# Performance work log

Hardware: AMD Instinct MI355X
Metric: run time of the kernel (lower is better)

Reference implementation:

```python
import jax, jax.numpy as jnp
import numpy as np
import math

B, H, S, D = 8, 16, 1024, 64

def setup_inputs() -> dict:
    key = jax.random.key(0)
    kq, kk, kv = jax.random.split(key, 3)
    Q = jax.random.normal(kq, (B, H, S, D), dtype=jnp.float32)
    K = jax.random.normal(kk, (B, H, S, D), dtype=jnp.float32)
    V = jax.random.normal(kv, (B, H, S, D), dtype=jnp.float32)
    return {"Q": Q, "K": K, "V": V}

def reference(Q, K, V):
    d_k = K.shape[-1]
    # [B,H,S,S] attention scores
    score = jnp.einsum('bhqd,bhkd->bhqk', Q, K) / math.sqrt(d_k)
    attn = jax.nn.softmax(score, axis=-1)
    return jnp.einsum('bhqk,bhkd->bhqd', attn, V)
```

## Files before the change

### kernel.cpp

```cpp
#include <hip/hip_runtime.h>
#include <hip/hip_bf16.h>
#include <math.h>


#define S_ 1024
#define D_ 64
#define BQ 256
#define KVT 64
#define NTILE (S_ / KVT)
#define TILE_SHORTS (KVT * D_)

typedef __attribute__((ext_vector_type(8))) short bf16x8;
typedef __attribute__((ext_vector_type(4))) float f32x4;

#if __has_builtin(__builtin_amdgcn_exp2f)
#define EXP2F(x) __builtin_amdgcn_exp2f(x)
#else
#define EXP2F(x) exp2f(x)
#endif

__device__ __forceinline__ short f2bf(float f) {
    union { __hip_bfloat16 h; short s; } u;
    u.h = __float2bfloat16(f);
    return u.s;
}

__device__ __forceinline__ unsigned int pkbf(float a, float b) {
    unsigned int ua = __float_as_uint(a) + 0x8000u;
    unsigned int ub = __float_as_uint(b) + 0x8000u;
    return __builtin_amdgcn_perm(ub, ua, 0x07060302u);
}

__launch_bounds__(256)
__global__ void prepass_kernel(const float* __restrict__ K, const float* __restrict__ V,
                               short* __restrict__ Kb, short* __restrict__ Vb) {
    __shared__ __align__(16) short VtL[D_][72];
    const int tile = blockIdx.x, bh = blockIdx.y;
    const int tid = threadIdx.x;
    const int kv0 = tile * KVT;
    const size_t base = (size_t)bh * (S_ * D_);
    const float* Kp = K + base;
    const float* Vp = V + base;
    short* Kt = Kb + ((size_t)bh * NTILE + tile) * TILE_SHORTS;
    short* Vt = Vb + ((size_t)bh * NTILE + tile) * TILE_SHORTS;

    {
        const int c4 = tid & 15, g = tid >> 4;
        #pragma unroll
        for (int i = 0; i < 2; ++i) {
            const int kp = g + 16 * i;
            #pragma unroll
            for (int j = 0; j < 4; ++j) {
                const int d = c4 + 16 * j;
                float v0 = Vp[(size_t)(kv0 + 2 * kp) * D_ + d];
                float v1 = Vp[(size_t)(kv0 + 2 * kp + 1) * D_ + d];
                short2 vs; vs.x = f2bf(v0); vs.y = f2bf(v1);
                *(short2*)&VtL[d][2 * kp] = vs;
            }
        }
    }
    #pragma unroll
    for (int i = 0; i < 2; ++i) {
        const int s = tid + i * 256;
        const int mb = s >> 7, c = (s >> 6) & 1, lane = s & 63;
        const int quad = lane >> 4, l16 = lane & 15;
        const float* src = Kp + (size_t)(kv0 + mb * 16 + l16) * D_ + c * 32 + quad * 8;
        float4 a = *(const float4*)src;
        float4 b = *(const float4*)(src + 4);
        bf16x8 f;
        f[0]=f2bf(a.x); f[1]=f2bf(a.y); f[2]=f2bf(a.z); f[3]=f2bf(a.w);
        f[4]=f2bf(b.x); f[5]=f2bf(b.y); f[6]=f2bf(b.z); f[7]=f2bf(b.w);
        *(bf16x8*)&Kt[s * 8] = f;
    }
    __syncthreads();
    #pragma unroll
    for (int i = 0; i < 2; ++i) {
        const int s = tid + i * 256;
        const int t = s >> 7, c = (s >> 6) & 1, lane = s & 63;
        const int quad = lane >> 4, l16 = lane & 15;
        bf16x8 f = *(const bf16x8*)&VtL[t * 16 + l16][c * 32 + quad * 8];
        *(bf16x8*)&Vt[s * 8] = f;
    }
}

__launch_bounds__(256, 2)
__global__ void sdpa_kernel(const float* __restrict__ Q,
                            const short* __restrict__ Kb,
                            const short* __restrict__ Vb,
                            float* __restrict__ O) {
    __shared__ __align__(16) short Pfrag[4][4][1024];

    const int b   = blockIdx.x;
    const int bh  = (b & 7) | ((b >> 5) << 3);
    const int q0  = ((b >> 3) & 3) * BQ;
    const int tid = threadIdx.x;
    const int w = tid >> 6, lane = tid & 63;
    const int quad = lane >> 4, l16 = lane & 15;

    const size_t base = (size_t)bh * (S_ * D_);
    const float* Qp = Q + base;
    float*       Op = O + base;
    const short* Kg = Kb + (size_t)bh * NTILE * TILE_SHORTS;
    const short* Vg = Vb + (size_t)bh * NTILE * TILE_SHORTS;

    const float qs = 0.18033688011112042f;
    bf16x8 qfrag[4][2];
    #pragma unroll
    for (int nb = 0; nb < 4; ++nb) {
        const int qrow = q0 + w * 64 + nb * 16 + l16;
        #pragma unroll
        for (int c = 0; c < 2; ++c) {
            const float* src = Qp + (size_t)qrow * D_ + c * 32 + quad * 8;
            float4 a = *(const float4*)(src);
            float4 bb = *(const float4*)(src + 4);
            bf16x8 f;
            f[0]=f2bf(a.x*qs);  f[1]=f2bf(a.y*qs);  f[2]=f2bf(a.z*qs);  f[3]=f2bf(a.w*qs);
            f[4]=f2bf(bb.x*qs); f[5]=f2bf(bb.y*qs); f[6]=f2bf(bb.z*qs); f[7]=f2bf(bb.w*qs);
            qfrag[nb][c] = f;
        }
    }

    bf16x8 ones;
    #pragma unroll
    for (int i = 0; i < 8; ++i) ones[i] = (short)0x3F80;

    f32x4 l_acc[4];
    f32x4 o_acc[4][4];
    #pragma unroll
    for (int nb = 0; nb < 4; ++nb) {
        l_acc[nb] = (f32x4)0.f;
        #pragma unroll
        for (int t4 = 0; t4 < 4; ++t4)
            o_acc[nb][t4] = (f32x4)0.f;
    }

    auto body = [&](bf16x8 (&kfc)[4][2], bf16x8 (&kfn)[4][2], int t) {
        bf16x8 vf[4][2];
        {
            const short* vt = Vg + (size_t)t * TILE_SHORTS;
            #pragma unroll
            for (int mb = 0; mb < 4; ++mb) {
                vf[mb][0] = *(const bf16x8*)(vt + ((mb * 2 + 0) * 64 + lane) * 8);
                vf[mb][1] = *(const bf16x8*)(vt + ((mb * 2 + 1) * 64 + lane) * 8);
            }
        }
        if (t + 1 < NTILE) {
            const short* kt = Kg + (size_t)(t + 1) * TILE_SHORTS;
            #pragma unroll
            for (int mb = 0; mb < 4; ++mb) {
                kfn[mb][0] = *(const bf16x8*)(kt + ((mb * 2 + 0) * 64 + lane) * 8);
                kfn[mb][1] = *(const bf16x8*)(kt + ((mb * 2 + 1) * 64 + lane) * 8);
            }
        }

        #pragma unroll
        for (int nb = 0; nb < 4; ++nb) {
            f32x4 st[4];
            #pragma unroll
            for (int mb = 0; mb < 4; ++mb) {
                f32x4 acc = (f32x4)0.f;
                acc = __builtin_amdgcn_mfma_f32_16x16x32_bf16(kfc[mb][0], qfrag[nb][0], acc, 0, 0, 0);
                acc = __builtin_amdgcn_mfma_f32_16x16x32_bf16(kfc[mb][1], qfrag[nb][1], acc, 0, 0, 0);
                st[mb] = acc;
            }

            #pragma unroll
            for (int mb = 0; mb < 4; ++mb) {
                float p0 = EXP2F(st[mb][0]);
                float p1 = EXP2F(st[mb][1]);
                float p2 = EXP2F(st[mb][2]);
                float p3 = EXP2F(st[mb][3]);
                uint2 pk;
                pk.x = pkbf(p0, p1);
                pk.y = pkbf(p2, p3);
                const int c  = mb >> 1;
                const int qp = (mb & 1) * 2 + (quad >> 1);
                const int j0 = (quad & 1) * 4;
                *(uint2*)&Pfrag[w][nb][(c * 64 + qp * 16 + l16) * 8 + j0] = pk;
            }
            bf16x8 pf0 = *(const bf16x8*)&Pfrag[w][nb][(0 * 64 + lane) * 8];
            bf16x8 pf1 = *(const bf16x8*)&Pfrag[w][nb][(1 * 64 + lane) * 8];

            l_acc[nb] = __builtin_amdgcn_mfma_f32_16x16x32_bf16(pf0, ones, l_acc[nb], 0, 0, 0);
            l_acc[nb] = __builtin_amdgcn_mfma_f32_16x16x32_bf16(pf1, ones, l_acc[nb], 0, 0, 0);

            #pragma unroll
            for (int t4 = 0; t4 < 4; ++t4) {
                f32x4 acc = o_acc[nb][t4];
                acc = __builtin_amdgcn_mfma_f32_16x16x32_bf16(pf0, vf[t4][0], acc, 0, 0, 0);
                acc = __builtin_amdgcn_mfma_f32_16x16x32_bf16(pf1, vf[t4][1], acc, 0, 0, 0);
                o_acc[nb][t4] = acc;
            }
        }
    };

    bf16x8 kfA[4][2], kfB[4][2];
    #pragma unroll
    for (int mb = 0; mb < 4; ++mb) {
        kfA[mb][0] = *(const bf16x8*)(Kg + ((mb * 2 + 0) * 64 + lane) * 8);
        kfA[mb][1] = *(const bf16x8*)(Kg + ((mb * 2 + 1) * 64 + lane) * 8);
    }

    #pragma unroll 1
    for (int tt = 0; tt < NTILE; tt += 2) {
        body(kfA, kfB, tt);
        body(kfB, kfA, tt + 1);
    }

    #pragma unroll
    for (int nb = 0; nb < 4; ++nb) {
        #pragma unroll
        for (int r = 0; r < 4; ++r) {
            const float inv = 1.0f / l_acc[nb][r];
            const int row = q0 + w * 64 + nb * 16 + quad * 4 + r;
            #pragma unroll
            for (int t4 = 0; t4 < 4; ++t4)
                Op[(size_t)row * D_ + t4 * 16 + l16] = o_acc[nb][t4][r] * inv;
        }
    }
}

extern "C" void kernel_launch(void* const* d_in, const int* in_sizes, int n_in,
                              void* d_out, int out_size, void* d_ws, size_t ws_size,
                              hipStream_t stream) {
    const float* Q = (const float*)d_in[0];
    const float* K = (const float*)d_in[1];
    const float* V = (const float*)d_in[2];
    float* O = (float*)d_out;

    const size_t tensor_shorts = (size_t)128 * NTILE * TILE_SHORTS;
    short* Kb = (short*)d_ws;
    short* Vb = Kb + tensor_shorts;

    dim3 pgrid(NTILE, 8 * 16);
    prepass_kernel<<<pgrid, dim3(256), 0, stream>>>(K, V, Kb, Vb);

    sdpa_kernel<<<dim3(512), dim3(256), 0, stream>>>(Q, Kb, Vb, O);
}
```

Baseline: 164.0 us.

## Switch attention to 32x32x16 MFMA with in-register P transpose via permlane32 swap

Moves the attention kernel from 16x16x32 to 32x32x16 bf16 MFMA tiles and re-lays out the prepacked K/V fragments to match. The P matrix is reshaped into the PV operand layout in registers with permlane32 swaps, removing the LDS round trip through Pfrag and the extra MFMA that computed row sums. Row sums are now accumulated with scalar adds and combined across half-waves at the end. It also drops the double-buffered K prefetch, so K and V for each tile are loaded at the start of that tile's iteration, which may expose more load latency.

```diff
diff --git a/kernel.cpp b/kernel.cpp
--- a/kernel.cpp
+++ b/kernel.cpp
@@ -11,7 +11,8 @@
 #define TILE_SHORTS (KVT * D_)
 
 typedef __attribute__((ext_vector_type(8))) short bf16x8;
-typedef __attribute__((ext_vector_type(4))) float f32x4;
+typedef __attribute__((ext_vector_type(16))) float f32x16;
+typedef __attribute__((ext_vector_type(4))) unsigned int ui4;
 
 #if __has_builtin(__builtin_amdgcn_exp2f)
 #define EXP2F(x) __builtin_amdgcn_exp2f(x)
@@ -29,6 +30,20 @@
     unsigned int ua = __float_as_uint(a) + 0x8000u;
     unsigned int ub = __float_as_uint(b) + 0x8000u;
     return __builtin_amdgcn_perm(ub, ua, 0x07060302u);
+}
+
+__device__ __forceinline__ void swap32(unsigned int x, unsigned int y,
+                                       unsigned int& lo, unsigned int& hi) {
+#if __has_builtin(__builtin_amdgcn_permlane32_swap)
+    auto r = __builtin_amdgcn_permlane32_swap(x, y, false, false);
+    lo = r[0]; hi = r[1];
+#else
+    const int h = (threadIdx.x >> 5) & 1;
+    unsigned int xs = (unsigned int)__shfl_xor((int)x, 32);
+    unsigned int ys = (unsigned int)__shfl_xor((int)y, 32);
+    lo = h ? ys : x;
+    hi = h ? y : xs;
+#endif
 }
 
 __launch_bounds__(256)
@@ -62,9 +77,9 @@
     #pragma unroll
     for (int i = 0; i < 2; ++i) {
         const int s = tid + i * 256;
-        const int mb = s >> 7, c = (s >> 6) & 1, lane = s & 63;
-        const int quad = lane >> 4, l16 = lane & 15;
-        const float* src = Kp + (size_t)(kv0 + mb * 16 + l16) * D_ + c * 32 + quad * 8;
+        const int mb = s >> 8, c = (s >> 6) & 3, lane = s & 63;
+        const int l32 = lane & 31, h = lane >> 5;
+        const float* src = Kp + (size_t)(kv0 + mb * 32 + l32) * D_ + 16 * c + 8 * h;
         float4 a = *(const float4*)src;
         float4 b = *(const float4*)(src + 4);
         bf16x8 f;
@@ -76,9 +91,9 @@
     #pragma unroll
     for (int i = 0; i < 2; ++i) {
         const int s = tid + i * 256;
-        const int t = s >> 7, c = (s >> 6) & 1, lane = s & 63;
-        const int quad = lane >> 4, l16 = lane & 15;
-        bf16x8 f = *(const bf16x8*)&VtL[t * 16 + l16][c * 32 + quad * 8];
+        const int nd = s >> 8, c = (s >> 6) & 3, lane = s & 63;
+        const int l32 = lane & 31, h = lane >> 5;
+        bf16x8 f = *(const bf16x8*)&VtL[nd * 32 + l32][16 * c + 8 * h];
         *(bf16x8*)&Vt[s * 8] = f;
     }
 }
@@ -88,14 +103,12 @@
                             const short* __restrict__ Kb,
                             const short* __restrict__ Vb,
                             float* __restrict__ O) {
-    __shared__ __align__(16) short Pfrag[4][4][1024];
-
     const int b   = blockIdx.x;
     const int bh  = (b & 7) | ((b >> 5) << 3);
     const int q0  = ((b >> 3) & 3) * BQ;
     const int tid = threadIdx.x;
     const int w = tid >> 6, lane = tid & 63;
-    const int quad = lane >> 4, l16 = lane & 15;
+    const int l32 = lane & 31, h = lane >> 5;
 
     const size_t base = (size_t)bh * (S_ * D_);
     const float* Qp = Q + base;
@@ -104,13 +117,13 @@
     const short* Vg = Vb + (size_t)bh * NTILE * TILE_SHORTS;
 
     const float qs = 0.18033688011112042f;
-    bf16x8 qfrag[4][2];
-    #pragma unroll
-    for (int nb = 0; nb < 4; ++nb) {
-        const int qrow = q0 + w * 64 + nb * 16 + l16;
-        #pragma unroll
-        for (int c = 0; c < 2; ++c) {
-            const float* src = Qp + (size_t)qrow * D_ + c * 32 + quad * 8;
+    bf16x8 qfrag[2][4];
+    #pragma unroll
+    for (int nb = 0; nb < 2; ++nb) {
+        const int qrow = q0 + w * 64 + nb * 32 + l32;
+        #pragma unroll
+        for (int c = 0; c < 4; ++c) {
+            const float* src = Qp + (size_t)qrow * D_ + 16 * c + 8 * h;
             float4 a = *(const float4*)(src);
             float4 bb = *(const float4*)(src + 4);
             bf16x8 f;
@@ -120,102 +133,92 @@
         }
     }
 
-    bf16x8 ones;
-    #pragma unroll
-    for (int i = 0; i < 8; ++i) ones[i] = (short)0x3F80;
-
-    f32x4 l_acc[4];
-    f32x4 o_acc[4][4];
-    #pragma unroll
-    for (int nb = 0; nb < 4; ++nb) {
-        l_acc[nb] = (f32x4)0.f;
-        #pragma unroll
-        for (int t4 = 0; t4 < 4; ++t4)
-            o_acc[nb][t4] = (f32x4)0.f;
-    }
-
-    auto body = [&](bf16x8 (&kfc)[4][2], bf16x8 (&kfn)[4][2], int t) {
-        bf16x8 vf[4][2];
-        {
-            const short* vt = Vg + (size_t)t * TILE_SHORTS;
-            #pragma unroll
-            for (int mb = 0; mb < 4; ++mb) {
-                vf[mb][0] = *(const bf16x8*)(vt + ((mb * 2 + 0) * 64 + lane) * 8);
-                vf[mb][1] = *(const bf16x8*)(vt + ((mb * 2 + 1) * 64 + lane) * 8);
-            }
-        }
-        if (t + 1 < NTILE) {
-            const short* kt = Kg + (size_t)(t + 1) * TILE_SHORTS;
-            #pragma unroll
-            for (int mb = 0; mb < 4; ++mb) {
-                kfn[mb][0] = *(const bf16x8*)(kt + ((mb * 2 + 0) * 64 + lane) * 8);
-                kfn[mb][1] = *(const bf16x8*)(kt + ((mb * 2 + 1) * 64 + lane) * 8);
-            }
-        }
-
-        #pragma unroll
-        for (int nb = 0; nb < 4; ++nb) {
-            f32x4 st[4];
-            #pragma unroll
-            for (int mb = 0; mb < 4; ++mb) {
-                f32x4 acc = (f32x4)0.f;
-                acc = __builtin_amdgcn_mfma_f32_16x16x32_bf16(kfc[mb][0], qfrag[nb][0], acc, 0, 0, 0);
-                acc = __builtin_amdgcn_mfma_f32_16x16x32_bf16(kfc[mb][1], qfrag[nb][1], acc, 0, 0, 0);
+    float l_half[2] = {0.f, 0.f};
+    f32x16 o_acc[2][2];
+    #pragma unroll
+    for (int nb = 0; nb < 2; ++nb)
+        #pragma unroll
+        for (int nd = 0; nd < 2; ++nd)
+            o_acc[nb][nd] = (f32x16)0.f;
+
+    #pragma unroll 1
+    for (int t = 0; t < NTILE; ++t) {
+        const short* kt = Kg + (size_t)t * TILE_SHORTS;
+        const short* vt = Vg + (size_t)t * TILE_SHORTS;
+        bf16x8 kf[2][4], vf[2][4];
+        #pragma unroll
+        for (int mb = 0; mb < 2; ++mb)
+            #pragma unroll
+            for (int c = 0; c < 4; ++c)
+                kf[mb][c] = *(const bf16x8*)(kt + (((mb * 4 + c) * 64) + lane) * 8);
+        #pragma unroll
+        for (int nd = 0; nd < 2; ++nd)
+            #pragma unroll
+            for (int c = 0; c < 4; ++c)
+                vf[nd][c] = *(const bf16x8*)(vt + (((nd * 4 + c) * 64) + lane) * 8);
+
+        #pragma unroll
+        for (int nb = 0; nb < 2; ++nb) {
+            f32x16 st[2];
+            #pragma unroll
+            for (int mb = 0; mb < 2; ++mb) {
+                f32x16 acc = (f32x16)0.f;
+                #pragma unroll
+                for (int c = 0; c < 4; ++c)
+                    acc = __builtin_amdgcn_mfma_f32_32x32x16_bf16(kf[mb][c], qfrag[nb][c], acc, 0, 0, 0);
                 st[mb] = acc;
             }
 
-            #pragma unroll
-            for (int mb = 0; mb < 4; ++mb) {
-                float p0 = EXP2F(st[mb][0]);
-                float p1 = EXP2F(st[mb][1]);
-                float p2 = EXP2F(st[mb][2]);
-                float p3 = EXP2F(st[mb][3]);
-                uint2 pk;
-                pk.x = pkbf(p0, p1);
-                pk.y = pkbf(p2, p3);
-                const int c  = mb >> 1;
-                const int qp = (mb & 1) * 2 + (quad >> 1);
-                const int j0 = (quad & 1) * 4;
-                *(uint2*)&Pfrag[w][nb][(c * 64 + qp * 16 + l16) * 8 + j0] = pk;
+            unsigned int E[2][4][2];
+            float lh = 0.f;
+            #pragma unroll
+            for (int mb = 0; mb < 2; ++mb)
+                #pragma unroll
+                for (int m4 = 0; m4 < 4; ++m4)
+                    #pragma unroll
+                    for (int u = 0; u < 2; ++u) {
+                        float p0 = EXP2F(st[mb][4 * m4 + 2 * u]);
+                        float p1 = EXP2F(st[mb][4 * m4 + 2 * u + 1]);
+                        lh += p0 + p1;
+                        E[mb][m4][u] = pkbf(p0, p1);
+                    }
+            l_half[nb] += lh;
+
+            bf16x8 pa[4];
+            #pragma unroll
+            for (int mb = 0; mb < 2; ++mb)
+                #pragma unroll
+                for (int cc = 0; cc < 2; ++cc) {
+                    unsigned int lo0, hi0, lo1, hi1;
+                    swap32(E[mb][2 * cc][0], E[mb][2 * cc + 1][0], lo0, hi0);
+                    swap32(E[mb][2 * cc][1], E[mb][2 * cc + 1][1], lo1, hi1);
+                    union { ui4 u; bf16x8 bf; } cv;
+                    cv.u = (ui4){lo0, lo1, hi0, hi1};
+                    pa[2 * mb + cc] = cv.bf;
+                }
+
+            #pragma unroll
+            for (int nd = 0; nd < 2; ++nd) {
+                f32x16 acc = o_acc[nb][nd];
+                #pragma unroll
+                for (int c = 0; c < 4; ++c)
+                    acc = __builtin_amdgcn_mfma_f32_32x32x16_bf16(pa[c], vf[nd][c], acc, 0, 0, 0);
+                o_acc[nb][nd] = acc;
             }
-            bf16x8 pf0 = *(const bf16x8*)&Pfrag[w][nb][(0 * 64 + lane) * 8];
-            bf16x8 pf1 = *(const bf16x8*)&Pfrag[w][nb][(1 * 64 + lane) * 8];
-
-            l_acc[nb] = __builtin_amdgcn_mfma_f32_16x16x32_bf16(pf0, ones, l_acc[nb], 0, 0, 0);
-            l_acc[nb] = __builtin_amdgcn_mfma_f32_16x16x32_bf16(pf1, ones, l_acc[nb], 0, 0, 0);
-
-            #pragma unroll
-            for (int t4 = 0; t4 < 4; ++t4) {
-                f32x4 acc = o_acc[nb][t4];
-                acc = __builtin_amdgcn_mfma_f32_16x16x32_bf16(pf0, vf[t4][0], acc, 0, 0, 0);
-                acc = __builtin_amdgcn_mfma_f32_16x16x32_bf16(pf1, vf[t4][1], acc, 0, 0, 0);
-                o_acc[nb][t4] = acc;
-            }
-        }
-    };
-
-    bf16x8 kfA[4][2], kfB[4][2];
-    #pragma unroll
-    for (int mb = 0; mb < 4; ++mb) {
-        kfA[mb][0] = *(const bf16x8*)(Kg + ((mb * 2 + 0) * 64 + lane) * 8);
-        kfA[mb][1] = *(const bf16x8*)(Kg + ((mb * 2 + 1) * 64 + lane) * 8);
-    }
-
-    #pragma unroll 1
-    for (int tt = 0; tt < NTILE; tt += 2) {
-        body(kfA, kfB, tt);
-        body(kfB, kfA, tt + 1);
-    }
-
-    #pragma unroll
-    for (int nb = 0; nb < 4; ++nb) {
-        #pragma unroll
-        for (int r = 0; r < 4; ++r) {
-            const float inv = 1.0f / l_acc[nb][r];
-            const int row = q0 + w * 64 + nb * 16 + quad * 4 + r;
-            #pragma unroll
-            for (int t4 = 0; t4 < 4; ++t4)
-                Op[(size_t)row * D_ + t4 * 16 + l16] = o_acc[nb][t4][r] * inv;
+        }
+    }
+
+    #pragma unroll
+    for (int nb = 0; nb < 2; ++nb) {
+        float lt  = l_half[nb] + __shfl_xor(l_half[nb], 32);
+        float inv = 1.0f / lt;
+        #pragma unroll
+        for (int r = 0; r < 16; ++r) {
+            const int ql   = (r & 3) + 8 * (r >> 2) + 4 * h;
+            const float iv = __shfl(inv, ql);
+            const int row  = q0 + w * 64 + nb * 32 + ql;
+            Op[(size_t)row * D_ + 0  + l32] = o_acc[nb][0][r] * iv;
+            Op[(size_t)row * D_ + 32 + l32] = o_acc[nb][1][r] * iv;
         }
     }
 }
```

Result: slower. 169.1 us (+3.1%).
